# Kernel tuning notes

Hardware: AMD Instinct MI355X
Metric: run time of the kernel (lower is better)

Reference implementation:

```python
import jax, jax.numpy as jnp
import numpy as np
from jax import lax

B, C, H, W = 16, 128, 128, 128
COUT, KH, KW, K, RED, TEMP = 128, 3, 3, 4, 4, 30.0
ATTN_CH = max(C // RED, 1)

def setup_inputs() -> dict:
    key = jax.random.key(0)
    ks = jax.random.split(key, 7)
    fan_out = COUT * KH * KW
    std = np.sqrt(2.0 / fan_out)  # kaiming_normal fan_out, relu
    return {
        "x": jax.random.normal(ks[0], (B, C, H, W), dtype=jnp.float32),
        "weight": jax.random.normal(ks[1], (K, COUT, C, KH, KW), dtype=jnp.float32) * std,
        "bias": jnp.zeros((K, COUT), dtype=jnp.float32),
        "aw1": jax.random.normal(ks[2], (ATTN_CH, C), dtype=jnp.float32) * (1.0 / np.sqrt(C)),
        "ab1": jnp.zeros((ATTN_CH,), dtype=jnp.float32),
        "aw2": jax.random.normal(ks[3], (K, ATTN_CH), dtype=jnp.float32) * (1.0 / np.sqrt(ATTN_CH)),
        "ab2": jnp.zeros((K,), dtype=jnp.float32),
    }

def reference(x, weight, bias, aw1, ab1, aw2, ab2):
    # Attention branch: global avg pool -> 1x1 conv -> relu -> 1x1 conv
    pooled = jnp.mean(x, axis=(2, 3))                       # (B, C)
    h = jax.nn.relu(pooled @ aw1.T + ab1)                   # (B, attn_ch)
    scores = h @ aw2.T + ab2                                # (B, K)
    attn = jax.nn.softmax(scores / TEMP, axis=1)            # (B, K)

    # Per-sample aggregated kernel and bias
    agg_w = jnp.einsum('bk,koipq->boipq', attn, weight)     # (B, Cout, Cin, kH, kW)
    agg_b = attn @ bias                                     # (B, Cout)

    # Per-sample conv2d (stride 1, padding 1, dilation 1, groups 1)
    def conv_one(xi, wi):
        return lax.conv_general_dilated(
            xi[None], wi,
            window_strides=(1, 1),
            padding=((1, 1), (1, 1)),
            dimension_numbers=('NCHW', 'OIHW', 'NCHW'),
        )[0]

    out = jax.vmap(conv_one)(x, agg_w)                      # (B, Cout, H, W)
    return out + agg_b[:, :, None, None]
```

## Files before the change

kernel.cpp:

```cpp
#include <hip/hip_runtime.h>

typedef float f32x4 __attribute__((ext_vector_type(4)));
typedef short bf16x8 __attribute__((ext_vector_type(8)));

__device__ __forceinline__ unsigned short f2bf(float f) {
  unsigned u = __builtin_bit_cast(unsigned, f);
  u = (u + 0x7FFFu + ((u >> 16) & 1u)) >> 16;
  return (unsigned short)u;
}

__device__ __forceinline__ void async16(const unsigned short* g, unsigned short* l) {
  __builtin_amdgcn_global_load_lds(
      (__attribute__((address_space(1))) void*)g,
      (__attribute__((address_space(3))) void*)l, 16, 0, 0);
}

#define XT_ROW 16640

__global__ __launch_bounds__(256) void k_transpose(const float* __restrict__ x,
                                                   unsigned short* __restrict__ xt,
                                                   float* __restrict__ rowsum) {
  __shared__ unsigned short tile[128][128];
  __shared__ float psum[128][8];
  const int y = blockIdx.x, b = blockIdx.y;
  const int t = threadIdx.x;
  const int colb = (t & 7) * 16;
  const int cp = t >> 3;
  const int swz = (t & 7) << 3;
  for (int ci = 0; ci < 4; ++ci) {
    const int c = ci * 32 + cp;
    const int c2 = c ^ swz;
    const float* src = x + (((size_t)(b * 128 + c) * 128 + y) * 128 + colb);
    float s = 0.f;
#pragma unroll
    for (int j = 0; j < 16; j += 4) {
      float4 v = *(const float4*)(src + j);
      s += v.x + v.y + v.z + v.w;
      tile[colb + j + 0][c2] = f2bf(v.x);
      tile[colb + j + 1][c2] = f2bf(v.y);
      tile[colb + j + 2][c2] = f2bf(v.z);
      tile[colb + j + 3][c2] = f2bf(v.w);
    }
    psum[c][t & 7] = s;
  }
  __syncthreads();
#pragma unroll
  for (int it = 0; it < 8; ++it) {
    const int slot = t + it * 256;
    const int col = slot >> 4;
    const int cg = (slot & 15) * 8;
    const int c2 = cg ^ (((col >> 4) & 7) << 3);
    uint4 vv = *(const uint4*)&tile[col][c2];
    *(uint4*)(xt + (((size_t)b * 130 + y + 1) * 130 + col + 1) * 128 + cg) = vv;
  }
  if (t < 128) {
    float r = 0.f;
#pragma unroll
    for (int j = 0; j < 8; ++j) r += psum[t][j];
    rowsum[((size_t)b * 128 + t) * 128 + y] = r;
  }
}

__global__ __launch_bounds__(256) void k_border(unsigned short* __restrict__ xt) {
  const int b = blockIdx.y;
  const int idx = blockIdx.x * 256 + threadIdx.x;
  if (idx >= 8256) return;
  int row, col, ck;
  if (idx < 4160) {
    row = (idx < 2080) ? 0 : 129;
    const int s = idx % 2080;
    col = s >> 4;
    ck = s & 15;
  } else {
    const int s = idx - 4160;
    row = (s >> 5) + 1;
    col = (s & 16) ? 129 : 0;
    ck = s & 15;
  }
  uint4 z = {0, 0, 0, 0};
  *(uint4*)(xt + ((size_t)b * 130 + row) * 130 * 128 + (size_t)col * 128 + ck * 8) = z;
}

__global__ __launch_bounds__(128) void k_attn(const float* __restrict__ rowsum,
                                              const float* __restrict__ aw1,
                                              const float* __restrict__ ab1,
                                              const float* __restrict__ aw2,
                                              const float* __restrict__ ab2,
                                              const float* __restrict__ bias,
                                              float* __restrict__ attn,
                                              float* __restrict__ aggb) {
  __shared__ float pooled[128];
  __shared__ float h[32];
  __shared__ float at[4];
  const int b = blockIdx.x, t = threadIdx.x;
  const float* rs = rowsum + (size_t)(b * 128 + t) * 128;
  float s = 0.f;
  for (int yy = 0; yy < 128; ++yy) s += rs[yy];
  pooled[t] = s * (1.f / 16384.f);
  __syncthreads();
  if (t < 32) {
    float hv = ab1[t];
    for (int c = 0; c < 128; ++c) hv += pooled[c] * aw1[t * 128 + c];
    h[t] = fmaxf(hv, 0.f);
  }
  __syncthreads();
  if (t < 4) {
    float sc = ab2[t];
    for (int a = 0; a < 32; ++a) sc += h[a] * aw2[t * 32 + a];
    at[t] = sc * (1.f / 30.f);
  }
  __syncthreads();
  if (t == 0) {
    float m = fmaxf(fmaxf(at[0], at[1]), fmaxf(at[2], at[3]));
    float e0 = __expf(at[0] - m), e1 = __expf(at[1] - m);
    float e2 = __expf(at[2] - m), e3 = __expf(at[3] - m);
    float inv = 1.f / (e0 + e1 + e2 + e3);
    at[0] = e0 * inv; at[1] = e1 * inv; at[2] = e2 * inv; at[3] = e3 * inv;
  }
  __syncthreads();
  if (t < 4) attn[b * 4 + t] = at[t];
  float ab = 0.f;
  for (int k = 0; k < 4; ++k) ab += at[k] * bias[k * 128 + t];
  aggb[b * 128 + t] = ab;
}

__global__ __launch_bounds__(256) void k_aggw(const float* __restrict__ weight,
                                              const float* __restrict__ attn,
                                              unsigned short* __restrict__ aggw) {
  const int fid = blockIdx.x * 256 + threadIdx.x;
  const int kk = fid & 31;
  const int o = (fid >> 5) & 127;
  const int rest = fid >> 12;
  const int s = rest % 36;
  const int b = rest / 36;
  const int c = ((s & 3) << 5) + kk;
  const int pq = s >> 2;
  const size_t src = (size_t)o * 1152 + (size_t)c * 9 + pq;
  float v = attn[b * 4 + 0] * weight[src]
          + attn[b * 4 + 1] * weight[src + 147456]
          + attn[b * 4 + 2] * weight[src + 2 * 147456]
          + attn[b * 4 + 3] * weight[src + 3 * 147456];
  aggw[fid] = f2bf(v);
}

__global__ __launch_bounds__(256, 3) void k_conv(const unsigned short* __restrict__ xt,
                                                 const unsigned short* __restrict__ aggw,
                                                 const float* __restrict__ aggb,
                                                 float* __restrict__ out) {
  __shared__ unsigned short lds[3][8192];
  const int id = blockIdx.x;
  const int swz = (id & 7) * 256 + (id >> 3);
  const int b = swz >> 7, y = swz & 127;
  const int t = threadIdx.x;
  const int lane = t & 63, w = t >> 6;
  const int mw = w >> 1, nw = w & 1;
  const int l15 = lane & 15, lk = lane >> 4;
  const int rswz = (l15 & 3) * 8;

  const unsigned short* aS[2];
  const unsigned short* bS[2];
  int dA[2], dB[2];
#pragma unroll
  for (int i = 0; i < 2; ++i) {
    const int c = i * 256 + t;
    const int n = c >> 2, k8 = c & 3;
    const int sk = (k8 ^ (n & 3)) * 8;
    aS[i] = aggw + (size_t)b * 147456 + n * 32 + sk;
    bS[i] = xt + ((size_t)(b * 130 + y) * 130 + n) * 128 + sk;
    dA[i] = i * 2048 + w * 512;
    dB[i] = 4096 + i * 2048 + w * 512;
  }

#define STAGE(buf, s) {                                                        \
    const int tap_ = (s) >> 2, c0_ = ((s) & 3) << 5;                           \
    const int p_ = tap_ / 3, q_ = tap_ - 3 * p_;                               \
    async16(aS[0] + (s) * 4096, &lds[buf][0] + dA[0]);                         \
    async16(aS[1] + (s) * 4096, &lds[buf][0] + dA[1]);                         \
    async16(bS[0] + p_ * XT_ROW + q_ * 128 + c0_, &lds[buf][0] + dB[0]);       \
    async16(bS[1] + p_ * XT_ROW + q_ * 128 + c0_, &lds[buf][0] + dB[1]);       \
  }

  f32x4 acc[4][4] = {};
  STAGE(0, 0);
  STAGE(1, 1);

#pragma unroll
  for (int s = 0; s < 36; ++s) {
    const int cur = s % 3;
    if (s < 35) { asm volatile("s_waitcnt vmcnt(4)" ::: "memory"); }
    else        { asm volatile("s_waitcnt vmcnt(0)" ::: "memory"); }
    __builtin_amdgcn_sched_barrier(0);
    __builtin_amdgcn_s_barrier();
    __builtin_amdgcn_sched_barrier(0);
    if (s + 2 < 36) STAGE((s + 2) % 3, s + 2);
    __builtin_amdgcn_sched_barrier(0);

    const unsigned short* A0 = &lds[cur][0];
    const unsigned short* B0 = &lds[cur][4096];
    bf16x8 af[4], bfr[4];
#pragma unroll
    for (int mi = 0; mi < 4; ++mi) {
      const int row = mw * 64 + mi * 16 + l15;
      af[mi] = *(const bf16x8*)(A0 + row * 32 + ((lk * 8) ^ rswz));
    }
#pragma unroll
    for (int ni = 0; ni < 4; ++ni) {
      const int row = nw * 64 + ni * 16 + l15;
      bfr[ni] = *(const bf16x8*)(B0 + row * 32 + ((lk * 8) ^ rswz));
    }
    __builtin_amdgcn_s_setprio(1);
#pragma unroll
    for (int mi = 0; mi < 4; ++mi)
#pragma unroll
      for (int ni = 0; ni < 4; ++ni)
        acc[mi][ni] = __builtin_amdgcn_mfma_f32_16x16x32_bf16(af[mi], bfr[ni], acc[mi][ni], 0, 0, 0);
    __builtin_amdgcn_s_setprio(0);
  }
#undef STAGE

  const int colb = nw * 64 + l15;
#pragma unroll
  for (int mi = 0; mi < 4; ++mi) {
    const int o = mw * 64 + mi * 16 + lk * 4;
#pragma unroll
    for (int rr = 0; rr < 4; ++rr) {
      const float bsv = aggb[b * 128 + o + rr];
      float* orow = out + ((size_t)(b * 128 + o + rr) * 128 + y) * 128 + colb;
      orow[0]  = acc[mi][0][rr] + bsv;
      orow[16] = acc[mi][1][rr] + bsv;
      orow[32] = acc[mi][2][rr] + bsv;
      orow[48] = acc[mi][3][rr] + bsv;
    }
  }
}

extern "C" void kernel_launch(void* const* d_in, const int* in_sizes, int n_in,
                              void* d_out, int out_size, void* d_ws, size_t ws_size,
                              hipStream_t stream) {
  const float* x      = (const float*)d_in[0];
  const float* weight = (const float*)d_in[1];
  const float* bias   = (const float*)d_in[2];
  const float* aw1    = (const float*)d_in[3];
  const float* ab1    = (const float*)d_in[4];
  const float* aw2    = (const float*)d_in[5];
  const float* ab2    = (const float*)d_in[6];
  float* out = (float*)d_out;

  char* ws = (char*)d_ws;
  unsigned short* xt   = (unsigned short*)ws;
  unsigned short* aggw = (unsigned short*)(ws + 69222400);
  float* rowsum        = (float*)(ws + 69222400 + 4718592);
  float* attn          = (float*)(ws + 69222400 + 4718592 + 1048576);
  float* aggb          = (float*)(ws + 69222400 + 4718592 + 1048576 + 256);

  hipLaunchKernelGGL(k_border, dim3(33, 16), dim3(256), 0, stream, xt);
  hipLaunchKernelGGL(k_transpose, dim3(128, 16), dim3(256), 0, stream, x, xt, rowsum);
  hipLaunchKernelGGL(k_attn, dim3(16), dim3(128), 0, stream,
                     rowsum, aw1, ab1, aw2, ab2, bias, attn, aggb);
  hipLaunchKernelGGL(k_aggw, dim3(9216), dim3(256), 0, stream, weight, attn, aggw);
  hipLaunchKernelGGL(k_conv, dim3(2048), dim3(256), 0, stream, xt, aggw, aggb, out);
}
```

Baseline: 149.7 us.

## Stage full input halo rows in LDS and compute two output rows per block

The conv kernel now computes two output rows per block with 512 threads. It loads the four padded input rows (4x130x128 bf16) into LDS once up front and reuses them across all 9 taps and channel chunks. Only the weight tiles are streamed through a triple buffer, instead of re-fetching a shifted input tile for every tap. This removes about 9x redundant global/L2 traffic for input pixels and shares each weight tile across two rows. In exchange it uses about 154KB of LDS per block, which limits occupancy and adds an upfront load latency that is not overlapped.

```diff
diff --git a/kernel.cpp b/kernel.cpp
--- a/kernel.cpp
+++ b/kernel.cpp
@@ -143,71 +143,79 @@
   aggw[fid] = f2bf(v);
 }
 
-__global__ __launch_bounds__(256, 3) void k_conv(const unsigned short* __restrict__ xt,
+__global__ __launch_bounds__(512, 2) void k_conv(const unsigned short* __restrict__ xt,
                                                  const unsigned short* __restrict__ aggw,
                                                  const float* __restrict__ aggb,
                                                  float* __restrict__ out) {
-  __shared__ unsigned short lds[3][8192];
+  __shared__ unsigned short lds[78848];
   const int id = blockIdx.x;
-  const int swz = (id & 7) * 256 + (id >> 3);
-  const int b = swz >> 7, y = swz & 127;
+  const int swz = (id & 7) * 128 + (id >> 3);
+  const int b = swz >> 6;
+  const int y0 = (swz & 63) * 2;
   const int t = threadIdx.x;
   const int lane = t & 63, w = t >> 6;
-  const int mw = w >> 1, nw = w & 1;
+  const int mw = w >> 2, nw = w & 3;
   const int l15 = lane & 15, lk = lane >> 4;
-  const int rswz = (l15 & 3) * 8;
-
-  const unsigned short* aS[2];
-  const unsigned short* bS[2];
-  int dA[2], dB[2];
-#pragma unroll
-  for (int i = 0; i < 2; ++i) {
-    const int c = i * 256 + t;
-    const int n = c >> 2, k8 = c & 3;
-    const int sk = (k8 ^ (n & 3)) * 8;
-    aS[i] = aggw + (size_t)b * 147456 + n * 32 + sk;
-    bS[i] = xt + ((size_t)(b * 130 + y) * 130 + n) * 128 + sk;
-    dA[i] = i * 2048 + w * 512;
-    dB[i] = 4096 + i * 2048 + w * 512;
-  }
-
-#define STAGE(buf, s) {                                                        \
-    const int tap_ = (s) >> 2, c0_ = ((s) & 3) << 5;                           \
-    const int p_ = tap_ / 3, q_ = tap_ - 3 * p_;                               \
-    async16(aS[0] + (s) * 4096, &lds[buf][0] + dA[0]);                         \
-    async16(aS[1] + (s) * 4096, &lds[buf][0] + dA[1]);                         \
-    async16(bS[0] + p_ * XT_ROW + q_ * 128 + c0_, &lds[buf][0] + dB[0]);       \
-    async16(bS[1] + p_ * XT_ROW + q_ * 128 + c0_, &lds[buf][0] + dB[1]);       \
-  }
-
+
+  {
+    const unsigned short* xb = xt + (size_t)(b * 130 + y0) * XT_ROW;
+#pragma unroll
+    for (int i = 0; i < 16; ++i) {
+      const int idx = i * 512 + t;
+      const int row = idx / 2080, rem = idx % 2080;
+      const int col = rem >> 4, k8 = rem & 15;
+      async16(xb + (row * 130 + col) * 128 + ((k8 ^ (col & 15)) * 8),
+              &lds[0] + i * 4096 + w * 512);
+    }
+    if (w < 2) {
+      const int idx = 8192 + t;
+      const int row = idx / 2080, rem = idx % 2080;
+      const int col = rem >> 4, k8 = rem & 15;
+      async16(xb + (row * 130 + col) * 128 + ((k8 ^ (col & 15)) * 8),
+              &lds[0] + 65536 + w * 512);
+    }
+  }
+  const int an = t >> 2, ak8 = t & 3;
+  const unsigned short* aS = aggw + (size_t)b * 147456 + an * 32
+                           + ((ak8 ^ ((an >> 1) & 3)) * 8);
+  unsigned short* aldsw = &lds[66560] + w * 512;
+
+#define STAGE_A(buf, s) async16(aS + (s) * 4096, aldsw + (buf) * 4096)
+
+  STAGE_A(0, 0);
+  STAGE_A(1, 1);
+
+  const int rbase = (nw >> 1) * 16640;
+  const int px0 = (nw & 1) * 64 + l15;
   f32x4 acc[4][4] = {};
-  STAGE(0, 0);
-  STAGE(1, 1);
 
 #pragma unroll
   for (int s = 0; s < 36; ++s) {
-    const int cur = s % 3;
-    if (s < 35) { asm volatile("s_waitcnt vmcnt(4)" ::: "memory"); }
+    const int tap = s >> 2, cc = s & 3;
+    const int p = tap / 3, q = tap - 3 * p;
+    if (s < 35) { asm volatile("s_waitcnt vmcnt(1)" ::: "memory"); }
     else        { asm volatile("s_waitcnt vmcnt(0)" ::: "memory"); }
     __builtin_amdgcn_sched_barrier(0);
     __builtin_amdgcn_s_barrier();
     __builtin_amdgcn_sched_barrier(0);
-    if (s + 2 < 36) STAGE((s + 2) % 3, s + 2);
-    __builtin_amdgcn_sched_barrier(0);
-
-    const unsigned short* A0 = &lds[cur][0];
-    const unsigned short* B0 = &lds[cur][4096];
+
+    const unsigned short* A0 = &lds[66560 + (s % 3) * 4096];
     bf16x8 af[4], bfr[4];
 #pragma unroll
     for (int mi = 0; mi < 4; ++mi) {
       const int row = mw * 64 + mi * 16 + l15;
-      af[mi] = *(const bf16x8*)(A0 + row * 32 + ((lk * 8) ^ rswz));
+      af[mi] = *(const bf16x8*)(A0 + row * 32 + ((lk ^ ((row >> 1) & 3)) * 8));
     }
 #pragma unroll
     for (int ni = 0; ni < 4; ++ni) {
-      const int row = nw * 64 + ni * 16 + l15;
-      bfr[ni] = *(const bf16x8*)(B0 + row * 32 + ((lk * 8) ^ rswz));
-    }
+      const int col = px0 + ni * 16 + q;
+      bfr[ni] = *(const bf16x8*)(&lds[0] + rbase + p * 16640 + col * 128
+                                 + (((cc * 4 + lk) ^ (col & 15)) * 8));
+    }
+    if (s + 2 < 36) STAGE_A((s + 2) % 3, s + 2);
+    __builtin_amdgcn_sched_barrier(0);
+    asm volatile("s_waitcnt lgkmcnt(0)" ::: "memory");
+    __builtin_amdgcn_sched_barrier(0);
     __builtin_amdgcn_s_setprio(1);
 #pragma unroll
     for (int mi = 0; mi < 4; ++mi)
@@ -215,10 +223,12 @@
       for (int ni = 0; ni < 4; ++ni)
         acc[mi][ni] = __builtin_amdgcn_mfma_f32_16x16x32_bf16(af[mi], bfr[ni], acc[mi][ni], 0, 0, 0);
     __builtin_amdgcn_s_setprio(0);
-  }
-#undef STAGE
-
-  const int colb = nw * 64 + l15;
+    __builtin_amdgcn_sched_barrier(0);
+  }
+#undef STAGE_A
+
+  const int y = y0 + (nw >> 1);
+  const int colb = (nw & 1) * 64 + l15;
 #pragma unroll
   for (int mi = 0; mi < 4; ++mi) {
     const int o = mw * 64 + mi * 16 + lk * 4;
@@ -258,5 +268,5 @@
   hipLaunchKernelGGL(k_attn, dim3(16), dim3(128), 0, stream,
                      rowsum, aw1, ab1, aw2, ab2, bias, attn, aggb);
   hipLaunchKernelGGL(k_aggw, dim3(9216), dim3(256), 0, stream, weight, attn, aggw);
-  hipLaunchKernelGGL(k_conv, dim3(2048), dim3(256), 0, stream, xt, aggw, aggb, out);
-}
+  hipLaunchKernelGGL(k_conv, dim3(1024), dim3(512), 0, stream, xt, aggw, aggb, out);
+}
```

After: 154.4 us. 1.03x slower.

## Switch conv pipeline to double buffering with new LDS swizzle and higher occupancy

Applied to the files above, without the earlier changes.

Replaces the three-stage LDS ring with two buffers. Each iteration now issues the next stage's async loads before computing on the current buffer, then waits for all loads and a barrier at the end of the step. LDS per block shrinks, so the launch-bounds hint rises to four blocks per CU, and the XOR swizzle now uses (row>>1)&3 to change the LDS bank-conflict pattern. The cost is a shallower prefetch, with a full vmcnt(0) wait every step that may expose load latency.

```diff
diff --git a/kernel.cpp b/kernel.cpp
--- a/kernel.cpp
+++ b/kernel.cpp
@@ -143,11 +143,11 @@
   aggw[fid] = f2bf(v);
 }
 
-__global__ __launch_bounds__(256, 3) void k_conv(const unsigned short* __restrict__ xt,
+__global__ __launch_bounds__(256, 4) void k_conv(const unsigned short* __restrict__ xt,
                                                  const unsigned short* __restrict__ aggw,
                                                  const float* __restrict__ aggb,
                                                  float* __restrict__ out) {
-  __shared__ unsigned short lds[3][8192];
+  __shared__ unsigned short lds[2][8192];
   const int id = blockIdx.x;
   const int swz = (id & 7) * 256 + (id >> 3);
   const int b = swz >> 7, y = swz & 127;
@@ -155,16 +155,17 @@
   const int lane = t & 63, w = t >> 6;
   const int mw = w >> 1, nw = w & 1;
   const int l15 = lane & 15, lk = lane >> 4;
-  const int rswz = (l15 & 3) * 8;
+  const int xc = (lk ^ ((l15 >> 1) & 3)) * 8;
+  const int aBase = mw * 2048 + l15 * 32 + xc;
+  const int bBase = 4096 + nw * 2048 + l15 * 32 + xc;
 
   const unsigned short* aS[2];
   const unsigned short* bS[2];
   int dA[2], dB[2];
 #pragma unroll
   for (int i = 0; i < 2; ++i) {
-    const int c = i * 256 + t;
-    const int n = c >> 2, k8 = c & 3;
-    const int sk = (k8 ^ (n & 3)) * 8;
+    const int c = i * 256 + t, n = c >> 2, k8 = c & 3;
+    const int sk = (k8 ^ ((n >> 1) & 3)) * 8;
     aS[i] = aggw + (size_t)b * 147456 + n * 32 + sk;
     bS[i] = xt + ((size_t)(b * 130 + y) * 130 + n) * 128 + sk;
     dA[i] = i * 2048 + w * 512;
@@ -182,39 +183,35 @@
 
   f32x4 acc[4][4] = {};
   STAGE(0, 0);
-  STAGE(1, 1);
+  asm volatile("s_waitcnt vmcnt(0)" ::: "memory");
+  __builtin_amdgcn_s_barrier();
 
 #pragma unroll
   for (int s = 0; s < 36; ++s) {
-    const int cur = s % 3;
-    if (s < 35) { asm volatile("s_waitcnt vmcnt(4)" ::: "memory"); }
-    else        { asm volatile("s_waitcnt vmcnt(0)" ::: "memory"); }
+    const int cur = s & 1;
+    if (s + 1 < 36) STAGE(cur ^ 1, s + 1);
+
+    const unsigned short* L = &lds[cur][0];
+    bf16x8 af[4], bfr[4];
+#pragma unroll
+    for (int mi = 0; mi < 4; ++mi)
+      af[mi] = *(const bf16x8*)(L + aBase + mi * 512);
+#pragma unroll
+    for (int ni = 0; ni < 4; ++ni)
+      bfr[ni] = *(const bf16x8*)(L + bBase + ni * 512);
+
+    __builtin_amdgcn_s_setprio(1);
+#pragma unroll
+    for (int mi = 0; mi < 4; ++mi)
+#pragma unroll
+      for (int ni = 0; ni < 4; ++ni)
+        acc[mi][ni] = __builtin_amdgcn_mfma_f32_16x16x32_bf16(af[mi], bfr[ni], acc[mi][ni], 0, 0, 0);
+    __builtin_amdgcn_s_setprio(0);
+
+    asm volatile("s_waitcnt vmcnt(0)" ::: "memory");
     __builtin_amdgcn_sched_barrier(0);
     __builtin_amdgcn_s_barrier();
     __builtin_amdgcn_sched_barrier(0);
-    if (s + 2 < 36) STAGE((s + 2) % 3, s + 2);
-    __builtin_amdgcn_sched_barrier(0);
-
-    const unsigned short* A0 = &lds[cur][0];
-    const unsigned short* B0 = &lds[cur][4096];
-    bf16x8 af[4], bfr[4];
-#pragma unroll
-    for (int mi = 0; mi < 4; ++mi) {
-      const int row = mw * 64 + mi * 16 + l15;
-      af[mi] = *(const bf16x8*)(A0 + row * 32 + ((lk * 8) ^ rswz));
-    }
-#pragma unroll
-    for (int ni = 0; ni < 4; ++ni) {
-      const int row = nw * 64 + ni * 16 + l15;
-      bfr[ni] = *(const bf16x8*)(B0 + row * 32 + ((lk * 8) ^ rswz));
-    }
-    __builtin_amdgcn_s_setprio(1);
-#pragma unroll
-    for (int mi = 0; mi < 4; ++mi)
-#pragma unroll
-      for (int ni = 0; ni < 4; ++ni)
-        acc[mi][ni] = __builtin_amdgcn_mfma_f32_16x16x32_bf16(af[mi], bfr[ni], acc[mi][ni], 0, 0, 0);
-    __builtin_amdgcn_s_setprio(0);
   }
 #undef STAGE
 
```

Result: slower. 155.1 us (+3.6%).
